# Performance work log

Measured on AMD Instinct MI355X. Metric: run time of the kernel, lower is better.

## Reference

```python
import jax, jax.numpy as jnp
import numpy as np

B, N, D, H, DH, PD = 2, 768, 512, 16, 32, 128
INNER = H * DH
NEG_INF = -10000.0
EPS = 1e-5


def _ln(x, w, b):
    m = jnp.mean(x, axis=-1, keepdims=True)
    v = jnp.mean((x - m) ** 2, axis=-1, keepdims=True)
    return (x - m) * jax.lax.rsqrt(v + EPS) * w + b


def setup_inputs() -> dict:
    key = jax.random.key(0)
    ks = jax.random.split(key, 8)
    s = 0.02
    return {
        "node_feats": jax.random.normal(ks[0], (B, N, D), jnp.float32),
        "pair_feats": jax.random.normal(ks[1], (B, N, N, PD), jnp.float32),
        "mask": jax.random.uniform(ks[2], (B, N, N)) > 0.1,
        "node_norm_w": jnp.ones((D,), jnp.float32),
        "node_norm_b": jnp.zeros((D,), jnp.float32),
        "qkv_w": jax.random.normal(ks[3], (D, 3 * INNER), jnp.float32) * s,
        "qkv_b": jnp.zeros((3 * INNER,), jnp.float32),
        "g_w": jax.random.normal(ks[4], (D, INNER), jnp.float32) * s,
        "g_b": jnp.zeros((INNER,), jnp.float32),
        "qln_w": jnp.ones((INNER,), jnp.float32),
        "qln_b": jnp.zeros((INNER,), jnp.float32),
        "kln_w": jnp.ones((INNER,), jnp.float32),
        "kln_b": jnp.zeros((INNER,), jnp.float32),
        "pair_norm_w": jnp.ones((PD,), jnp.float32),
        "pair_norm_b": jnp.zeros((PD,), jnp.float32),
        "bias_w": jax.random.normal(ks[5], (PD, H), jnp.float32) * s,
        "out_w": jax.random.normal(ks[6], (INNER, D), jnp.float32) * s,
        "out_b": jnp.zeros((D,), jnp.float32),
    }


def reference(node_feats, pair_feats, mask, node_norm_w, node_norm_b, qkv_w, qkv_b,
              g_w, g_b, qln_w, qln_b, kln_w, kln_b, pair_norm_w, pair_norm_b,
              bias_w, out_w, out_b):
    x = _ln(node_feats, node_norm_w, node_norm_b)              # (b,n,D)
    qkv = x @ qkv_w + qkv_b                                    # (b,n,3*inner)
    q, k, v = jnp.split(qkv, 3, axis=-1)
    q = _ln(q, qln_w, qln_b)                                   # QK-norm over inner_dim
    k = _ln(k, kln_w, kln_b)
    g = x @ g_w + g_b

    def heads(t):
        return t.reshape(B, N, H, DH).transpose(0, 2, 1, 3)    # b h n d

    q, k, v, g = map(heads, (q, k, v, g))

    pb = _ln(pair_feats, pair_norm_w, pair_norm_b)             # (b,i,j,PD)
    bias = jnp.einsum('bije,eh->bhij', pb, bias_w)             # (b,h,i,j)
    bias = jnp.where(mask[:, None, :, :], bias, NEG_INF)

    scale = 1.0 / np.sqrt(DH).astype(np.float32)
    scores = jnp.einsum('bhid,bhjd->bhij', q, k) * scale + bias
    attn = jax.nn.softmax(scores, axis=-1)
    o = jnp.einsum('bhij,bhjd->bhid', attn, v)
    o = jax.nn.sigmoid(g) * o                                  # sigmoid gating
    o = o.transpose(0, 2, 1, 3).reshape(B, N, INNER)
    return o @ out_w + out_b
```

## Files before the change

kernel.cpp:

```cpp
#include <hip/hip_runtime.h>
#include <hip/hip_bf16.h>
#include <math.h>

#define BB 2
#define NN 768
#define DD 512
#define HH 16
#define DHH 32
#define PDD 128
#define ROWS (BB*NN)

#define WC_OFF   0L
#define C12_OFF  2048L
#define X_OFF    4096L
#define QKV_OFF  (X_OFF    + 786432L)
#define GSIG_OFF (QKV_OFF  + 2359296L)
#define QN_OFF   (GSIG_OFF + 786432L)
#define KN_OFF   (QN_OFF   + 786432L)
#define OB_OFF   (KN_OFF   + 786432L)
#define BIAS_OFF (OB_OFF   + 786432L)

__global__ __launch_bounds__(256) void k_prep(const float* __restrict__ pnw,
                                              const float* __restrict__ pnb,
                                              const float* __restrict__ bw,
                                              float* __restrict__ ws) {
    int t = threadIdx.x;
    for (int idx = t; idx < 2048; idx += 256)
        ws[WC_OFF + idx] = pnw[idx >> 4] * bw[idx];
    if (t < 16) {
        float a = 0.f, b = 0.f;
        for (int e = 0; e < 128; e++) { a += pnb[e] * bw[e*16 + t]; b += pnw[e] * bw[e*16 + t]; }
        ws[C12_OFF + t] = a;
        ws[C12_OFF + 16 + t] = b;
    }
}

__global__ __launch_bounds__(256) void k_ln512(const float* __restrict__ in, long ld, long col0,
                                               const float* __restrict__ w, const float* __restrict__ bp,
                                               float* __restrict__ out) {
    int r = blockIdx.x, t = threadIdx.x;
    const float* src = in + (long)r * ld + col0;
    float v0 = src[t], v1 = src[t + 256];
    float s1 = v0 + v1, s2 = v0*v0 + v1*v1;
    __shared__ float red[16];
    #pragma unroll
    for (int off = 32; off > 0; off >>= 1) {
        s1 += __shfl_down(s1, off, 64);
        s2 += __shfl_down(s2, off, 64);
    }
    int wid = t >> 6, lane = t & 63;
    if (lane == 0) { red[wid] = s1; red[wid + 4] = s2; }
    __syncthreads();
    if (t == 0) {
        float a = red[0]+red[1]+red[2]+red[3];
        float c = red[4]+red[5]+red[6]+red[7];
        float mean = a / 512.f;
        float var  = c / 512.f - mean*mean;
        red[8] = mean; red[9] = rsqrtf(var + 1e-5f);
    }
    __syncthreads();
    float mean = red[8], rstd = red[9];
    out[(long)r*512 + t]       = (v0 - mean) * rstd * w[t]       + bp[t];
    out[(long)r*512 + t + 256] = (v1 - mean) * rstd * w[t + 256] + bp[t + 256];
}

__global__ __launch_bounds__(256) void k_qkvg(const float* __restrict__ x,
                                              const float* __restrict__ qkv_w, const float* __restrict__ qkv_b,
                                              const float* __restrict__ g_w,  const float* __restrict__ g_b,
                                              float* __restrict__ qkv_o, float* __restrict__ gsig) {
    __shared__ float As[16][64];
    __shared__ float Bs[16][64];
    int bx = blockIdx.x, by = blockIdx.y, t = threadIdx.x;
    bool isg = (bx >= 24);
    const float* Wp = isg ? g_w : qkv_w;
    const float* bp = isg ? g_b : qkv_b;
    long ldw = isg ? 512 : 1536;
    int c0 = isg ? (bx - 24) * 64 : bx * 64;
    int tr = t >> 4, tc = t & 15;
    int am = t >> 2, ak = (t & 3) * 4;
    int bk = t >> 4, bc = (t & 15) * 4;
    const float* xrow = x + (long)(by*64 + am)*512 + ak;
    float acc[4][4] = {};
    for (int kt = 0; kt < 32; kt++) {
        float4 av = *(const float4*)(xrow + kt*16);
        float4 bv = *(const float4*)(Wp + (long)(kt*16 + bk)*ldw + c0 + bc);
        As[ak+0][am] = av.x; As[ak+1][am] = av.y; As[ak+2][am] = av.z; As[ak+3][am] = av.w;
        *(float4*)&Bs[bk][bc] = bv;
        __syncthreads();
        #pragma unroll
        for (int k = 0; k < 16; k++) {
            float4 a4 = *(const float4*)&As[k][tr*4];
            float4 b4 = *(const float4*)&Bs[k][tc*4];
            float ar[4] = {a4.x, a4.y, a4.z, a4.w};
            float br[4] = {b4.x, b4.y, b4.z, b4.w};
            #pragma unroll
            for (int r = 0; r < 4; r++)
                #pragma unroll
                for (int c = 0; c < 4; c++)
                    acc[r][c] = fmaf(ar[r], br[c], acc[r][c]);
        }
        __syncthreads();
    }
    #pragma unroll
    for (int r = 0; r < 4; r++) {
        int row = by*64 + tr*4 + r;
        #pragma unroll
        for (int c = 0; c < 4; c++) {
            int col = c0 + tc*4 + c;
            float val = acc[r][c] + bp[col];
            if (!isg) qkv_o[(long)row*1536 + col] = val;
            else      gsig[(long)row*512 + col] = 1.f / (1.f + __expf(-val));
        }
    }
}

__global__ __launch_bounds__(256) void k_bias(const float* __restrict__ pair,
                                              const int* __restrict__ mask,
                                              const float* __restrict__ wsbase,
                                              float* __restrict__ bias_o) {
    __shared__ float pb[128 * 130];
    __shared__ float stats_m[128];
    __shared__ float stats_r[128];
    __shared__ float wc[2048];
    __shared__ float c12[32];
    int bid = blockIdx.x, t = threadIdx.x;
    int jt = bid % 6;
    int i  = (bid / 6) % 768;
    int b  = bid / (6 * 768);
    for (int idx = t; idx < 2048; idx += 256) wc[idx] = wsbase[WC_OFF + idx];
    if (t < 32) c12[t] = wsbase[C12_OFF + t];
    const float* src = pair + ((long)(b*NN + i)*NN + jt*128) * 128;
    for (int it = 0; it < 16; it++) {
        int f = t + it * 256;
        int j = f >> 5, c = f & 31;
        float4 v = *(const float4*)(src + (long)f * 4);
        float s1 = v.x + v.y + v.z + v.w;
        float s2 = v.x*v.x + v.y*v.y + v.z*v.z + v.w*v.w;
        #pragma unroll
        for (int off = 16; off > 0; off >>= 1) {
            s1 += __shfl_down(s1, off, 32);
            s2 += __shfl_down(s2, off, 32);
        }
        if (c == 0) {
            float mean = s1 / 128.f;
            float var  = s2 / 128.f - mean*mean;
            stats_m[j] = mean;
            stats_r[j] = rsqrtf(var + 1e-5f);
        }
        int rot = (j >> 2) * 2;
        int e0 = (c*4 + rot) & 127;
        int eb = (e0 + 2) & 127;
        int base = j * 130;
        *(float2*)&pb[base + e0] = make_float2(v.x, v.y);
        *(float2*)&pb[base + eb] = make_float2(v.z, v.w);
    }
    __syncthreads();
    int jr = t >> 3, hr = (t >> 1) & 3, ec = t & 1;
    const float* pr[4];
    #pragma unroll
    for (int jj = 0; jj < 4; jj++) pr[jj] = &pb[(jr*4 + jj) * 130];
    int rot = jr * 2;
    float acc[4][4] = {};
    int es = (ec*64 + rot) & 127;
    #pragma unroll
    for (int e2 = 0; e2 < 32; e2++) {
        int e = ec*64 + e2*2;
        float4 wa = *(const float4*)&wc[e*16 + hr*4];
        float4 wb = *(const float4*)&wc[e*16 + 16 + hr*4];
        float war[4] = {wa.x, wa.y, wa.z, wa.w};
        float wbr[4] = {wb.x, wb.y, wb.z, wb.w};
        #pragma unroll
        for (int jj = 0; jj < 4; jj++) {
            float2 pv = *(const float2*)&pr[jj][es];
            #pragma unroll
            for (int hh = 0; hh < 4; hh++)
                acc[jj][hh] = fmaf(pv.x, war[hh], fmaf(pv.y, wbr[hh], acc[jj][hh]));
        }
        es = (es + 2) & 127;
    }
    #pragma unroll
    for (int jj = 0; jj < 4; jj++)
        #pragma unroll
        for (int hh = 0; hh < 4; hh++)
            acc[jj][hh] += __shfl_xor(acc[jj][hh], 1, 64);
    if (ec == 0) {
        long mbase = (long)(b*NN + i)*NN + jt*128 + jr*4;
        int4 mk4 = *(const int4*)&mask[mbase];
        int mks[4] = {mk4.x, mk4.y, mk4.z, mk4.w};
        float rs4[4], rm4[4];
        #pragma unroll
        for (int jj = 0; jj < 4; jj++) {
            int j = jr*4 + jj;
            rs4[jj] = stats_r[j];
            rm4[jj] = stats_r[j] * stats_m[j];
        }
        #pragma unroll
        for (int hh = 0; hh < 4; hh++) {
            int h = hr*4 + hh;
            float c2h = c12[16 + h], c1h = c12[h];
            float vals[4];
            #pragma unroll
            for (int jj = 0; jj < 4; jj++)
                vals[jj] = mks[jj] ? (rs4[jj] * acc[jj][hh] - rm4[jj] * c2h + c1h) : -10000.f;
            float4 ov = make_float4(vals[0], vals[1], vals[2], vals[3]);
            *(float4*)&bias_o[((long)(b*16 + h)*NN + i)*NN + jt*128 + jr*4] = ov;
        }
    }
}

__global__ __launch_bounds__(128) void k_attn(const float* __restrict__ qn,
                                              const float* __restrict__ kn,
                                              const float* __restrict__ qkv,
                                              const float* __restrict__ gsig,
                                              const float* __restrict__ bias,
                                              float* __restrict__ obuf) {
    __shared__ float Ks[64][36];
    __shared__ float Vs[64][36];
    int it = blockIdx.x, bh = blockIdx.y;
    int b = bh >> 4, h = bh & 15;
    int t = threadIdx.x;
    int rg = t >> 4, s = t & 15;
    int i0 = it*16 + rg*2;
    const float* qp = qn + ((long)(b*NN) + i0)*512 + h*32;
    float4 q0[8], q1[8];
    #pragma unroll
    for (int c = 0; c < 8; c++) {
        q0[c] = ((const float4*)qp)[c];
        q1[c] = ((const float4*)(qp + 512))[c];
    }
    float m0 = -1e30f, m1 = -1e30f, l0 = 0.f, l1 = 0.f;
    float4 o0[8], o1[8];
    #pragma unroll
    for (int c = 0; c < 8; c++) { o0[c] = make_float4(0,0,0,0); o1[c] = make_float4(0,0,0,0); }
    const long bias0 = ((long)bh*NN + i0)*NN;
    const float scale = 0.17677669529663687f;

    for (int jt = 0; jt < 12; jt++) {
        int j0 = jt*64;
        __syncthreads();
        #pragma unroll
        for (int k = 0; k < 4; k++) {
            int f = t + k*128;
            int row = f >> 3, ch = (f & 7)*4;
            *(float4*)&Ks[row][ch] = *(const float4*)(kn  + ((long)(b*NN) + j0 + row)*512  + h*32 + ch);
            *(float4*)&Vs[row][ch] = *(const float4*)(qkv + ((long)(b*NN) + j0 + row)*1536 + 1024 + h*32 + ch);
        }
        __syncthreads();
        #pragma unroll
        for (int st = 0; st < 4; st++) {
            int j = s + st*16;
            float d0 = 0.f, d1 = 0.f;
            #pragma unroll
            for (int c = 0; c < 8; c++) {
                float4 kv = *(const float4*)&Ks[j][c*4];
                d0 = fmaf(kv.x, q0[c].x, d0); d0 = fmaf(kv.y, q0[c].y, d0);
                d0 = fmaf(kv.z, q0[c].z, d0); d0 = fmaf(kv.w, q0[c].w, d0);
                d1 = fmaf(kv.x, q1[c].x, d1); d1 = fmaf(kv.y, q1[c].y, d1);
                d1 = fmaf(kv.z, q1[c].z, d1); d1 = fmaf(kv.w, q1[c].w, d1);
            }
            float b0v = bias[bias0 + j0 + j];
            float b1v = bias[bias0 + NN + j0 + j];
            float s0 = fmaf(d0, scale, b0v);
            float s1 = fmaf(d1, scale, b1v);
            float mn0 = fmaxf(m0, s0), mn1 = fmaxf(m1, s1);
            float p0 = __expf(s0 - mn0), p1 = __expf(s1 - mn1);
            if (__any((s0 > m0) || (s1 > m1))) {
                float c0 = __expf(m0 - mn0), c1 = __expf(m1 - mn1);
                l0 = l0*c0 + p0; l1 = l1*c1 + p1;
                m0 = mn0; m1 = mn1;
                #pragma unroll
                for (int c = 0; c < 8; c++) {
                    float4 vv = *(const float4*)&Vs[j][c*4];
                    o0[c].x = fmaf(o0[c].x, c0, p0*vv.x); o0[c].y = fmaf(o0[c].y, c0, p0*vv.y);
                    o0[c].z = fmaf(o0[c].z, c0, p0*vv.z); o0[c].w = fmaf(o0[c].w, c0, p0*vv.w);
                    o1[c].x = fmaf(o1[c].x, c1, p1*vv.x); o1[c].y = fmaf(o1[c].y, c1, p1*vv.y);
                    o1[c].z = fmaf(o1[c].z, c1, p1*vv.z); o1[c].w = fmaf(o1[c].w, c1, p1*vv.w);
                }
            } else {
                l0 += p0; l1 += p1;
                #pragma unroll
                for (int c = 0; c < 8; c++) {
                    float4 vv = *(const float4*)&Vs[j][c*4];
                    o0[c].x = fmaf(p0, vv.x, o0[c].x); o0[c].y = fmaf(p0, vv.y, o0[c].y);
                    o0[c].z = fmaf(p0, vv.z, o0[c].z); o0[c].w = fmaf(p0, vv.w, o0[c].w);
                    o1[c].x = fmaf(p1, vv.x, o1[c].x); o1[c].y = fmaf(p1, vv.y, o1[c].y);
                    o1[c].z = fmaf(p1, vv.z, o1[c].z); o1[c].w = fmaf(p1, vv.w, o1[c].w);
                }
            }
        }
    }
    #pragma unroll
    for (int mk = 1; mk < 16; mk <<= 1) {
        float mo0 = __shfl_xor(m0, mk, 64), mo1 = __shfl_xor(m1, mk, 64);
        float lo0 = __shfl_xor(l0, mk, 64), lo1 = __shfl_xor(l1, mk, 64);
        float nm0 = fmaxf(m0, mo0), nm1 = fmaxf(m1, mo1);
        float a0 = __expf(m0 - nm0), b0 = __expf(mo0 - nm0);
        float a1 = __expf(m1 - nm1), b1 = __expf(mo1 - nm1);
        l0 = l0*a0 + lo0*b0; l1 = l1*a1 + lo1*b1;
        m0 = nm0; m1 = nm1;
        #pragma unroll
        for (int c = 0; c < 8; c++) {
            float4 t0, t1;
            t0.x = __shfl_xor(o0[c].x, mk, 64); t0.y = __shfl_xor(o0[c].y, mk, 64);
            t0.z = __shfl_xor(o0[c].z, mk, 64); t0.w = __shfl_xor(o0[c].w, mk, 64);
            t1.x = __shfl_xor(o1[c].x, mk, 64); t1.y = __shfl_xor(o1[c].y, mk, 64);
            t1.z = __shfl_xor(o1[c].z, mk, 64); t1.w = __shfl_xor(o1[c].w, mk, 64);
            o0[c].x = fmaf(t0.x, b0, o0[c].x*a0); o0[c].y = fmaf(t0.y, b0, o0[c].y*a0);
            o0[c].z = fmaf(t0.z, b0, o0[c].z*a0); o0[c].w = fmaf(t0.w, b0, o0[c].w*a0);
            o1[c].x = fmaf(t1.x, b1, o1[c].x*a1); o1[c].y = fmaf(t1.y, b1, o1[c].y*a1);
            o1[c].z = fmaf(t1.z, b1, o1[c].z*a1); o1[c].w = fmaf(t1.w, b1, o1[c].w*a1);
        }
    }
    int rsel = s >> 3, cs = s & 7;
    float4 a0 = o0[0], a1 = o1[0];
    #pragma unroll
    for (int k = 1; k < 8; k++) {
        bool c = (cs == k);
        a0.x = c ? o0[k].x : a0.x; a0.y = c ? o0[k].y : a0.y;
        a0.z = c ? o0[k].z : a0.z; a0.w = c ? o0[k].w : a0.w;
        a1.x = c ? o1[k].x : a1.x; a1.y = c ? o1[k].y : a1.y;
        a1.z = c ? o1[k].z : a1.z; a1.w = c ? o1[k].w : a1.w;
    }
    float4 ov;
    ov.x = rsel ? a1.x : a0.x; ov.y = rsel ? a1.y : a0.y;
    ov.z = rsel ? a1.z : a0.z; ov.w = rsel ? a1.w : a0.w;
    float inv = 1.f / (rsel ? l1 : l0);
    long base = ((long)(b*NN) + i0 + rsel)*512 + h*32 + cs*4;
    float4 g = *(const float4*)(gsig + base);
    float4 r;
    r.x = g.x * ov.x * inv; r.y = g.y * ov.y * inv;
    r.z = g.z * ov.z * inv; r.w = g.w * ov.w * inv;
    *(float4*)(obuf + base) = r;
}

__global__ __launch_bounds__(256) void k_out(const float* __restrict__ ob,
                                             const float* __restrict__ w,
                                             const float* __restrict__ bp,
                                             float* __restrict__ out) {
    __shared__ float As[16][64];
    __shared__ float Bs[16][64];
    int bx = blockIdx.x, by = blockIdx.y, t = threadIdx.x;
    int c0 = bx * 64;
    int tr = t >> 4, tc = t & 15;
    int am = t >> 2, ak = (t & 3) * 4;
    int bk = t >> 4, bc = (t & 15) * 4;
    const float* xrow = ob + (long)(by*64 + am)*512 + ak;
    float acc[4][4] = {};
    for (int kt = 0; kt < 32; kt++) {
        float4 av = *(const float4*)(xrow + kt*16);
        float4 bv = *(const float4*)(w + (long)(kt*16 + bk)*512 + c0 + bc);
        As[ak+0][am] = av.x; As[ak+1][am] = av.y; As[ak+2][am] = av.z; As[ak+3][am] = av.w;
        *(float4*)&Bs[bk][bc] = bv;
        __syncthreads();
        #pragma unroll
        for (int k = 0; k < 16; k++) {
            float4 a4 = *(const float4*)&As[k][tr*4];
            float4 b4 = *(const float4*)&Bs[k][tc*4];
            float ar[4] = {a4.x, a4.y, a4.z, a4.w};
            float br[4] = {b4.x, b4.y, b4.z, b4.w};
            #pragma unroll
            for (int r = 0; r < 4; r++)
                #pragma unroll
                for (int c = 0; c < 4; c++)
                    acc[r][c] = fmaf(ar[r], br[c], acc[r][c]);
        }
        __syncthreads();
    }
    #pragma unroll
    for (int r = 0; r < 4; r++) {
        int row = by*64 + tr*4 + r;
        #pragma unroll
        for (int c = 0; c < 4; c++) {
            int col = c0 + tc*4 + c;
            out[(long)row*512 + col] = acc[r][c] + bp[col];
        }
    }
}

extern "C" void kernel_launch(void* const* d_in, const int* in_sizes, int n_in,
                              void* d_out, int out_size, void* d_ws, size_t ws_size,
                              hipStream_t stream) {
    const float* node_feats = (const float*)d_in[0];
    const float* pair_feats = (const float*)d_in[1];
    const int*   mask       = (const int*)d_in[2];
    const float* node_w     = (const float*)d_in[3];
    const float* node_b     = (const float*)d_in[4];
    const float* qkv_w      = (const float*)d_in[5];
    const float* qkv_b      = (const float*)d_in[6];
    const float* g_w        = (const float*)d_in[7];
    const float* g_b        = (const float*)d_in[8];
    const float* qln_w      = (const float*)d_in[9];
    const float* qln_b      = (const float*)d_in[10];
    const float* kln_w      = (const float*)d_in[11];
    const float* kln_b      = (const float*)d_in[12];
    const float* pnw        = (const float*)d_in[13];
    const float* pnb        = (const float*)d_in[14];
    const float* bias_w     = (const float*)d_in[15];
    const float* out_w      = (const float*)d_in[16];
    const float* out_b      = (const float*)d_in[17];
    float* out = (float*)d_out;
    float* ws  = (float*)d_ws;

    float* x_buf    = ws + X_OFF;
    float* qkv_buf  = ws + QKV_OFF;
    float* gsig_buf = ws + GSIG_OFF;
    float* qn_buf   = ws + QN_OFF;
    float* kn_buf   = ws + KN_OFF;
    float* ob_buf   = ws + OB_OFF;
    float* bias_buf = ws + BIAS_OFF;

    k_prep<<<1, 256, 0, stream>>>(pnw, pnb, bias_w, ws);
    k_ln512<<<ROWS, 256, 0, stream>>>(node_feats, 512, 0, node_w, node_b, x_buf);
    k_qkvg<<<dim3(32, 24), 256, 0, stream>>>(x_buf, qkv_w, qkv_b, g_w, g_b, qkv_buf, gsig_buf);
    k_ln512<<<ROWS, 256, 0, stream>>>(qkv_buf, 1536, 0,   qln_w, qln_b, qn_buf);
    k_ln512<<<ROWS, 256, 0, stream>>>(qkv_buf, 1536, 512, kln_w, kln_b, kn_buf);
    k_bias<<<BB * 768 * 6, 256, 0, stream>>>(pair_feats, mask, ws, bias_buf);
    k_attn<<<dim3(48, 32), 128, 0, stream>>>(qn_buf, kn_buf, qkv_buf, gsig_buf, bias_buf, ob_buf);
    k_out<<<dim3(8, 24), 256, 0, stream>>>(ob_buf, out_w, out_b, out);
}
```

Measured before the change: 1.201 ms.

## Restructure pair-bias kernel to per-thread row processing without shared staging

The pair-bias kernel now has each thread own two consecutive (i,j) pair rows. It streams their 128 features straight from global memory, accumulates LayerNorm statistics and all 16 head projections in registers, and reads the folded weights from shared memory. This drops the shared-memory tile of pair features, the shuffle reductions and a sync, which cuts LDS traffic and instruction overhead. The cost is a strided per-thread global access pattern (each thread reads 512 contiguous bytes, so lanes in a wavefront are far apart), higher register pressure from 32 accumulators, and fewer blocks in flight.

```diff
diff --git a/kernel.cpp b/kernel.cpp
--- a/kernel.cpp
+++ b/kernel.cpp
@@ -118,93 +118,69 @@
                                               const int* __restrict__ mask,
                                               const float* __restrict__ wsbase,
                                               float* __restrict__ bias_o) {
-    __shared__ float pb[128 * 130];
-    __shared__ float stats_m[128];
-    __shared__ float stats_r[128];
-    __shared__ float wc[2048];
-    __shared__ float c12[32];
-    int bid = blockIdx.x, t = threadIdx.x;
-    int jt = bid % 6;
-    int i  = (bid / 6) % 768;
-    int b  = bid / (6 * 768);
-    for (int idx = t; idx < 2048; idx += 256) wc[idx] = wsbase[WC_OFF + idx];
-    if (t < 32) c12[t] = wsbase[C12_OFF + t];
-    const float* src = pair + ((long)(b*NN + i)*NN + jt*128) * 128;
-    for (int it = 0; it < 16; it++) {
-        int f = t + it * 256;
-        int j = f >> 5, c = f & 31;
-        float4 v = *(const float4*)(src + (long)f * 4);
-        float s1 = v.x + v.y + v.z + v.w;
-        float s2 = v.x*v.x + v.y*v.y + v.z*v.z + v.w*v.w;
-        #pragma unroll
-        for (int off = 16; off > 0; off >>= 1) {
-            s1 += __shfl_down(s1, off, 32);
-            s2 += __shfl_down(s2, off, 32);
-        }
-        if (c == 0) {
-            float mean = s1 / 128.f;
-            float var  = s2 / 128.f - mean*mean;
-            stats_m[j] = mean;
-            stats_r[j] = rsqrtf(var + 1e-5f);
-        }
-        int rot = (j >> 2) * 2;
-        int e0 = (c*4 + rot) & 127;
-        int eb = (e0 + 2) & 127;
-        int base = j * 130;
-        *(float2*)&pb[base + e0] = make_float2(v.x, v.y);
-        *(float2*)&pb[base + eb] = make_float2(v.z, v.w);
-    }
+    __shared__ float wcs[2048];
+    __shared__ float c12s[32];
+    int t = threadIdx.x;
+    for (int idx = t; idx < 2048; idx += 256) wcs[idx] = wsbase[WC_OFF + idx];
+    if (t < 32) c12s[t] = wsbase[C12_OFF + t];
     __syncthreads();
-    int jr = t >> 3, hr = (t >> 1) & 3, ec = t & 1;
-    const float* pr[4];
-    #pragma unroll
-    for (int jj = 0; jj < 4; jj++) pr[jj] = &pb[(jr*4 + jj) * 130];
-    int rot = jr * 2;
-    float acc[4][4] = {};
-    int es = (ec*64 + rot) & 127;
-    #pragma unroll
-    for (int e2 = 0; e2 < 32; e2++) {
-        int e = ec*64 + e2*2;
-        float4 wa = *(const float4*)&wc[e*16 + hr*4];
-        float4 wb = *(const float4*)&wc[e*16 + 16 + hr*4];
-        float war[4] = {wa.x, wa.y, wa.z, wa.w};
-        float wbr[4] = {wb.x, wb.y, wb.z, wb.w};
-        #pragma unroll
-        for (int jj = 0; jj < 4; jj++) {
-            float2 pv = *(const float2*)&pr[jj][es];
+
+    long g  = (long)blockIdx.x * 256 + t;
+    long r0 = g * 2;
+    const float4* p0 = (const float4*)pair + r0 * 32;
+
+    float acc0[16] = {}, acc1[16] = {};
+    float s0 = 0.f, q0 = 0.f, s1 = 0.f, q1 = 0.f;
+
+    #pragma unroll 4
+    for (int k = 0; k < 32; k++) {
+        float4 a = p0[k];
+        float4 b = p0[32 + k];
+        float ae[4] = {a.x, a.y, a.z, a.w};
+        float be[4] = {b.x, b.y, b.z, b.w};
+        const float* wr = &wcs[k * 64];
+        #pragma unroll
+        for (int e = 0; e < 4; e++) {
+            float pa = ae[e], pb = be[e];
+            s0 += pa; q0 = fmaf(pa, pa, q0);
+            s1 += pb; q1 = fmaf(pb, pb, q1);
             #pragma unroll
-            for (int hh = 0; hh < 4; hh++)
-                acc[jj][hh] = fmaf(pv.x, war[hh], fmaf(pv.y, wbr[hh], acc[jj][hh]));
-        }
-        es = (es + 2) & 127;
-    }
-    #pragma unroll
-    for (int jj = 0; jj < 4; jj++)
-        #pragma unroll
-        for (int hh = 0; hh < 4; hh++)
-            acc[jj][hh] += __shfl_xor(acc[jj][hh], 1, 64);
-    if (ec == 0) {
-        long mbase = (long)(b*NN + i)*NN + jt*128 + jr*4;
-        int4 mk4 = *(const int4*)&mask[mbase];
-        int mks[4] = {mk4.x, mk4.y, mk4.z, mk4.w};
-        float rs4[4], rm4[4];
-        #pragma unroll
-        for (int jj = 0; jj < 4; jj++) {
-            int j = jr*4 + jj;
-            rs4[jj] = stats_r[j];
-            rm4[jj] = stats_r[j] * stats_m[j];
-        }
-        #pragma unroll
-        for (int hh = 0; hh < 4; hh++) {
-            int h = hr*4 + hh;
-            float c2h = c12[16 + h], c1h = c12[h];
-            float vals[4];
-            #pragma unroll
-            for (int jj = 0; jj < 4; jj++)
-                vals[jj] = mks[jj] ? (rs4[jj] * acc[jj][hh] - rm4[jj] * c2h + c1h) : -10000.f;
-            float4 ov = make_float4(vals[0], vals[1], vals[2], vals[3]);
-            *(float4*)&bias_o[((long)(b*16 + h)*NN + i)*NN + jt*128 + jr*4] = ov;
-        }
+            for (int h4 = 0; h4 < 4; h4++) {
+                float4 w = *(const float4*)&wr[e * 16 + h4 * 4];
+                acc0[h4*4+0] = fmaf(pa, w.x, acc0[h4*4+0]);
+                acc0[h4*4+1] = fmaf(pa, w.y, acc0[h4*4+1]);
+                acc0[h4*4+2] = fmaf(pa, w.z, acc0[h4*4+2]);
+                acc0[h4*4+3] = fmaf(pa, w.w, acc0[h4*4+3]);
+                acc1[h4*4+0] = fmaf(pb, w.x, acc1[h4*4+0]);
+                acc1[h4*4+1] = fmaf(pb, w.y, acc1[h4*4+1]);
+                acc1[h4*4+2] = fmaf(pb, w.z, acc1[h4*4+2]);
+                acc1[h4*4+3] = fmaf(pb, w.w, acc1[h4*4+3]);
+            }
+        }
+    }
+
+    float mean0 = s0 * (1.f/128.f), mean1 = s1 * (1.f/128.f);
+    float var0 = q0 * (1.f/128.f) - mean0*mean0;
+    float var1 = q1 * (1.f/128.f) - mean1*mean1;
+    float rs0 = rsqrtf(var0 + 1e-5f), rs1 = rsqrtf(var1 + 1e-5f);
+    float rm0 = rs0 * mean0, rm1 = rs1 * mean1;
+
+    int2 mk = *(const int2*)&mask[r0];
+
+    int  j0 = (int)(r0 % 768);
+    long ri = r0 / 768;
+    long b  = ri / 768;
+    long i  = ri - b * 768;
+    long obase = ((b * 16) * 768 + i) * 768 + j0;
+
+    #pragma unroll
+    for (int h = 0; h < 16; h++) {
+        float c1h = c12s[h], c2h = c12s[16 + h];
+        float base = fmaf(-rm0, c2h, c1h);
+        float v0 = mk.x ? fmaf(rs0, acc0[h], base) : -10000.f;
+        float base1 = fmaf(-rm1, c2h, c1h);
+        float v1 = mk.y ? fmaf(rs1, acc1[h], base1) : -10000.f;
+        *(float2*)&bias_o[obase + (long)h * (768L*768L)] = make_float2(v0, v1);
     }
 }
 
@@ -414,7 +390,7 @@
     k_qkvg<<<dim3(32, 24), 256, 0, stream>>>(x_buf, qkv_w, qkv_b, g_w, g_b, qkv_buf, gsig_buf);
     k_ln512<<<ROWS, 256, 0, stream>>>(qkv_buf, 1536, 0,   qln_w, qln_b, qn_buf);
     k_ln512<<<ROWS, 256, 0, stream>>>(qkv_buf, 1536, 512, kln_w, kln_b, kn_buf);
-    k_bias<<<BB * 768 * 6, 256, 0, stream>>>(pair_feats, mask, ws, bias_buf);
+    k_bias<<<2304, 256, 0, stream>>>(pair_feats, mask, ws, bias_buf);
     k_attn<<<dim3(48, 32), 128, 0, stream>>>(qn_buf, kn_buf, qkv_buf, gsig_buf, bias_buf, ob_buf);
     k_out<<<dim3(8, 24), 256, 0, stream>>>(ob_buf, out_w, out_b, out);
 }
```

After: 1.041 ms. -13.3%, faster.
